# Kernel optimization log

Measured on AMD Instinct MI355X. Metric: run time of the kernel, lower is better.

The kernel has to match this reference:

```python
import jax, jax.numpy as jnp
import numpy as np

B, L, D_MODEL, D_MEM = 4, 8192, 512, 512
SSM_DIM = D_MODEL + D_MEM


def setup_inputs() -> dict:
    key = jax.random.key(0)
    ks = jax.random.split(key, 4)
    s = 0.02
    return {
        "x": jax.random.normal(ks[0], (B, L, D_MODEL), dtype=jnp.float32),
        "W_av": jax.random.normal(ks[1], (4 * D_MEM, D_MODEL), dtype=jnp.float32) * s,
        "b_av": jnp.zeros((4 * D_MEM,), dtype=jnp.float32),
        "W_go": jax.random.normal(ks[2], (D_MODEL, SSM_DIM), dtype=jnp.float32) * s,
        "b_go": jnp.zeros((D_MODEL,), dtype=jnp.float32),
        "W_out": jax.random.normal(ks[3], (2 * D_MODEL, D_MODEL), dtype=jnp.float32) * s,
        "b_out": jnp.zeros((2 * D_MODEL,), dtype=jnp.float32),
    }


def reference(x, W_av, b_av, W_go, b_go, W_out, b_out):
    d = D_MEM
    b = x.shape[0]
    # alpha_v = Linear(d_model -> 4*d_memory) on x[:, :-1]
    av = jnp.einsum("bld,kd->blk", x[:, :-1], W_av) + b_av
    # NRU memory update: alpha+*v+ - alpha-*v-  (all nonlins default to identity)
    ms_inp = av[..., :d] * av[..., d:2 * d] - av[..., 2 * d:3 * d] * av[..., 3 * d:4 * d]
    # associative cumsum scan along length, prefixed with zero initial memory
    ms = jnp.cumsum(ms_inp, axis=1)
    m_init = jnp.zeros((b, 1, d), dtype=x.dtype)
    ms = jnp.concatenate([m_init, ms], axis=1)  # [b, L, d_memory]
    ssm_inp = jnp.concatenate([x, ms], axis=2)  # [b, L, ssm_dim]
    # SSM sublayer (external registry module) stubbed as identity
    ssm_out = ssm_inp
    y = jnp.einsum("blk,dk->bld", ssm_out, W_go) + b_go  # gated_out
    y = jax.nn.gelu(y, approximate=False)  # activation='gelu' (torch exact erf)
    z = jnp.einsum("bld,kd->blk", y, W_out) + b_out  # [b, L, 2*d_model]
    y = z[..., :D_MODEL] * jax.nn.sigmoid(z[..., D_MODEL:])
    return y
```

## Files before the change

### kernel.cpp

```cpp
#include <hip/hip_runtime.h>
#include <hip/hip_bf16.h>
#include <math.h>

#define B_SZ 4
#define L_SZ 8192
#define DM 512
#define DMEM 512
#define M1 (B_SZ * (L_SZ - 1))
#define M2 (B_SZ * L_SZ)

typedef _Float16 h16;
typedef __attribute__((ext_vector_type(2))) _Float16 f16x2;
typedef __attribute__((ext_vector_type(8))) _Float16 f16x8;
typedef __attribute__((ext_vector_type(4))) float f32x4;

#define MFMA16(a, b, c) __builtin_amdgcn_mfma_f32_16x16x32_f16((a), (b), (c), 0, 0, 0)
#define WAVES_EU(mn, mx) __attribute__((amdgpu_waves_per_eu(mn, mx)))

__device__ __forceinline__ void gl16(const void* g, void* l) {
    __builtin_amdgcn_global_load_lds(
        (const __attribute__((address_space(1))) void*)g,
        (__attribute__((address_space(3))) void*)l, 16, 0, 0);
}

__device__ __forceinline__ f16x8 lds_frag(const h16* base, int row, int col, int key) {
    return *(const f16x8*)((const char*)base + row * 128 + ((col * 2) ^ (key << 4)));
}

__device__ __forceinline__ void xcd_remap(int& bx, int& by) {
    int gx = gridDim.x, gy = gridDim.y;
    int nwg = gx * gy;
    int lin = blockIdx.y * gx + blockIdx.x;
    int chunk = nwg >> 3;
    int l = (lin & 7) * chunk + (lin >> 3);
    by = l % gy;
    bx = l / gy;
}

__global__ __launch_bounds__(256) void conv_x(
    const float* __restrict__ src, h16* __restrict__ dst)
{
    int i = blockIdx.x * 256 + threadIdx.x;
    int m = i >> 6, bb = i & 63;
    const float4* s = (const float4*)(src + (size_t)m * 512 + bb * 8);
    float4 v0 = s[0], v1 = s[1];
    float vv[8] = {v0.x, v0.y, v0.z, v0.w, v1.x, v1.y, v1.z, v1.w};
    f16x8 o;
    #pragma unroll
    for (int j = 0; j < 8; ++j) o[j] = (h16)vv[j];
    int db = bb ^ (m & 7);
    *(f16x8*)(dst + (size_t)m * 512 + db * 8) = o;
}

__global__ __launch_bounds__(256) void pack_weights(
    const float* __restrict__ Wgo, const float* __restrict__ Wav,
    const float* __restrict__ Wout, h16* __restrict__ Wgoh,
    h16* __restrict__ Wavh, h16* __restrict__ Wouth)
{
    int i = blockIdx.x * 256 + threadIdx.x;
    const float* s;
    h16* d;
    if (i < 65536) {
        int r = i >> 7, bb = i & 127;
        s = Wgo + (size_t)r * 1024 + bb * 8;
        d = Wgoh + (size_t)r * 1024 + (bb ^ (r & 7)) * 8;
    } else if (i < 196608) {
        int j = i - 65536;
        int P = j >> 6, bb = j & 63;
        int by = P >> 7, lo = P & 127;
        int half = lo >> 6, g = (lo >> 4) & 3, nl = lo & 15;
        int orig = g * 512 + by * 32 + half * 16 + nl;
        s = Wav + (size_t)orig * 512 + bb * 8;
        d = Wavh + (size_t)P * 512 + (bb ^ (P & 7)) * 8;
    } else {
        int j = i - 196608;
        int P = j >> 6, bb = j & 63;
        int by = P >> 7, lo = P & 127;
        int chunk = lo >> 5, g = (lo >> 4) & 1, nl = lo & 15;
        int orig = g * 512 + by * 64 + chunk * 16 + nl;
        s = Wout + (size_t)orig * 512 + bb * 8;
        d = Wouth + (size_t)P * 512 + (bb ^ (P & 7)) * 8;
    }
    const float4* sv = (const float4*)s;
    float4 v0 = sv[0], v1 = sv[1];
    float vv[8] = {v0.x, v0.y, v0.z, v0.w, v1.x, v1.y, v1.z, v1.w};
    f16x8 hh;
    #pragma unroll
    for (int j = 0; j < 8; ++j) hh[j] = (h16)vv[j];
    *(f16x8*)d = hh;
}

#define PIPE_WAIT(N) do { \
    asm volatile("s_waitcnt vmcnt(" #N ")" ::: "memory"); \
    __builtin_amdgcn_s_barrier(); \
    asm volatile("" ::: "memory"); \
} while (0)
#define PIPE_POST() do { \
    __builtin_amdgcn_s_barrier(); \
    asm volatile("" ::: "memory"); \
} while (0)

__global__ __launch_bounds__(256) WAVES_EU(2, 2) void gemm_av_mfma(
    const h16* __restrict__ xh, const h16* __restrict__ Wh,
    const float* __restrict__ bav, float* __restrict__ ms_inp)
{
    __shared__ __align__(16) h16 As[2][128 * 64];
    __shared__ __align__(16) h16 Bh[2][128 * 64];

    int bx, by; xcd_remap(bx, by);
    const int tid = threadIdx.x, lane = tid & 63, w = tid >> 6;
    const int wm = (w & 1) * 64, wn = (w >> 1) * 64;
    const int bm = bx * 128;
    const int ln = lane & 15, ko = (lane >> 4) * 8;
    const int kb = ln & 7;
    const int wb = w * 1024;

    const char *aP[4], *hP[4];
    {
        const int r8 = lane >> 3, c16 = (lane & 7) * 16;
        #pragma unroll
        for (int i = 0; i < 4; ++i) {
            int row = i * 32 + w * 8 + r8;
            int mg = bm + row; if (mg > M1 - 1) mg = M1 - 1;
            size_t xr = (size_t)mg + (unsigned)mg / (L_SZ - 1);
            aP[i] = (const char*)xh + xr * (DM * 2) + c16;
            size_t br = (size_t)(by * 128 + row) * (DM * 2) + c16;
            hP[i] = (const char*)Wh + br;
        }
    }
    int ka[4];
    #pragma unroll
    for (int fm = 0; fm < 4; ++fm) {
        int m = bm + wm + fm * 16 + ln;
        int mg = m > M1 - 1 ? M1 - 1 : m;
        ka[fm] = (int)((mg + (unsigned)mg / (L_SZ - 1)) & 7);
    }

    f32x4 acc[4][4];
    #pragma unroll
    for (int i = 0; i < 4; ++i)
        #pragma unroll
        for (int j = 0; j < 4; ++j) acc[i][j] = (f32x4){0.f, 0.f, 0.f, 0.f};

#define STAGE_AV(koff, sel) do { \
    char* dA = (char*)As[sel]; char* dB = (char*)Bh[sel]; \
    gl16(aP[0] + (koff), dA + 0 * 4096 + wb); gl16(hP[0] + (koff), dB + 0 * 4096 + wb); \
    gl16(aP[1] + (koff), dA + 1 * 4096 + wb); gl16(hP[1] + (koff), dB + 1 * 4096 + wb); \
    gl16(aP[2] + (koff), dA + 2 * 4096 + wb); gl16(hP[2] + (koff), dB + 2 * 4096 + wb); \
    gl16(aP[3] + (koff), dA + 3 * 4096 + wb); gl16(hP[3] + (koff), dB + 3 * 4096 + wb); \
} while (0)

    STAGE_AV(0, 0);
    STAGE_AV(128, 1);
    for (int kt = 0; kt < 8; ++kt) {
        if (kt < 7) PIPE_WAIT(8); else PIPE_WAIT(0);
        const h16* A = As[kt & 1];
        const h16* B = Bh[kt & 1];
        #pragma unroll
        for (int s = 0; s < 2; ++s) {
            const int c = s * 32 + ko;
            f16x8 a[4];
            #pragma unroll
            for (int fm = 0; fm < 4; ++fm)
                a[fm] = lds_frag(A, wm + fm * 16 + ln, c, ka[fm]);
            #pragma unroll
            for (int fn = 0; fn < 4; ++fn) {
                f16x8 vh = lds_frag(B, wn + fn * 16 + ln, c, kb);
                #pragma unroll
                for (int fm = 0; fm < 4; ++fm)
                    acc[fm][fn] = MFMA16(a[fm], vh, acc[fm][fn]);
            }
        }
        PIPE_POST();
        if (kt + 2 < 8) STAGE_AV((kt + 2) * 128, kt & 1);
    }
#undef STAGE_AV

    const int lm = (lane >> 4) * 4;
    const int nn = by * 32 + (wn >> 6) * 16 + ln;
    const float b0 = bav[nn], b1 = bav[nn + 512], b2 = bav[nn + 1024], b3 = bav[nn + 1536];
    #pragma unroll
    for (int fm = 0; fm < 4; ++fm) {
        #pragma unroll
        for (int i = 0; i < 4; ++i) {
            int m = bm + wm + fm * 16 + lm + i;
            if (m < M1) {
                float a0 = acc[fm][0][i] + b0;
                float a1 = acc[fm][1][i] + b1;
                float a2 = acc[fm][2][i] + b2;
                float a3 = acc[fm][3][i] + b3;
                ms_inp[(size_t)m * DMEM + nn] = a0 * a1 - a2 * a3;
            }
        }
    }
}

__global__ __launch_bounds__(256) void scan_pass1(
    const float* __restrict__ ms_inp, float* __restrict__ csum)
{
    int c = blockIdx.x, b = blockIdx.y;
    int l0 = c * 128;
    int len = min(128, (L_SZ - 1) - l0);
    int t = threadIdx.x;
    const float2* p = (const float2*)(ms_inp + ((size_t)b * (L_SZ - 1) + l0) * DMEM) + t;
    float2 s = make_float2(0.f, 0.f);
    for (int i = 0; i < len; ++i) {
        float2 v = p[(size_t)i * 256];
        s.x += v.x; s.y += v.y;
    }
    ((float2*)(csum + ((size_t)b * 64 + c) * DMEM))[t] = s;
}

__global__ __launch_bounds__(256) void scan_pass2(float* __restrict__ csum)
{
    int sid = blockIdx.x * 4 + (threadIdx.x >> 6);
    int lane = threadIdx.x & 63;
    int b = sid >> 9, d = sid & 511;
    float* p = csum + (size_t)b * 64 * DMEM + d;
    float v = p[(size_t)lane * DMEM];
    #pragma unroll
    for (int off = 1; off < 64; off <<= 1) {
        float t = __shfl_up(v, off, 64);
        if (lane >= off) v += t;
    }
    float ex = __shfl_up(v, 1, 64);
    if (lane == 0) ex = 0.f;
    p[(size_t)lane * DMEM] = ex;
}

__global__ __launch_bounds__(256) void scan_pass3(
    const float* __restrict__ ms_inp, const float* __restrict__ csum,
    h16* __restrict__ msh)
{
    int c = blockIdx.x, b = blockIdx.y;
    int l0 = c * 128;
    int len = min(128, (L_SZ - 1) - l0);
    int t = threadIdx.x;
    float2 run = ((const float2*)(csum + ((size_t)b * 64 + c) * DMEM))[t];
    const float2* p = (const float2*)(ms_inp + ((size_t)b * (L_SZ - 1) + l0) * DMEM) + t;
    const int bb = t >> 2;
    const int sub = (t & 3) * 4;
    if (c == 0) {
        f16x2 z = {(h16)0.f, (h16)0.f};
        *(f16x2*)((char*)(msh + (size_t)b * L_SZ * DMEM) + bb * 16 + sub) = z;
    }
    for (int i = 0; i < len; ++i) {
        float2 v = p[(size_t)i * 256];
        run.x += v.x; run.y += v.y;
        int m = b * L_SZ + l0 + 1 + i;
        int db = bb ^ (m & 7);
        f16x2 o = {(h16)run.x, (h16)run.y};
        *(f16x2*)((char*)(msh + (size_t)m * DMEM) + db * 16 + sub) = o;
    }
}

__global__ __launch_bounds__(256) WAVES_EU(2, 2) void gemm_go_mfma(
    const h16* __restrict__ xh, const h16* __restrict__ msh,
    const h16* __restrict__ Wh,
    const float* __restrict__ bgo, h16* __restrict__ yh)
{
    __shared__ __align__(16) h16 As[2][128 * 64];
    __shared__ __align__(16) h16 Bh[2][128 * 64];

    int bx, by; xcd_remap(bx, by);
    const int tid = threadIdx.x, lane = tid & 63, w = tid >> 6;
    const int wm = (w & 1) * 64, wn = (w >> 1) * 64;
    const int bm = bx * 128, bn = by * 128;
    const int ln = lane & 15, ko = (lane >> 4) * 8;
    const int kk = ln & 7;
    const int wb = w * 1024;

    const char *xP[4], *mP[4], *hP[4];
    {
        const int r8 = lane >> 3, c16 = (lane & 7) * 16;
        #pragma unroll
        for (int i = 0; i < 4; ++i) {
            int row = i * 32 + w * 8 + r8;
            size_t ar = (size_t)(bm + row) * (DM * 2) + c16;
            xP[i] = (const char*)xh + ar;
            mP[i] = (const char*)msh + ar;
            size_t br = (size_t)(bn + row) * (2 * DM * 2) + c16;
            hP[i] = (const char*)Wh + br;
        }
    }

    f32x4 acc[4][4];
    #pragma unroll
    for (int i = 0; i < 4; ++i)
        #pragma unroll
        for (int j = 0; j < 4; ++j) acc[i][j] = (f32x4){0.f, 0.f, 0.f, 0.f};

#define STAGE_GO(tt, sel) do { \
    char* dA = (char*)As[sel]; char* dB = (char*)Bh[sel]; \
    const int bo = (tt) * 128; \
    if ((tt) < 8) { \
        const int ao = (tt) * 128; \
        gl16(xP[0] + ao, dA + 0 * 4096 + wb); gl16(hP[0] + bo, dB + 0 * 4096 + wb); \
        gl16(xP[1] + ao, dA + 1 * 4096 + wb); gl16(hP[1] + bo, dB + 1 * 4096 + wb); \
        gl16(xP[2] + ao, dA + 2 * 4096 + wb); gl16(hP[2] + bo, dB + 2 * 4096 + wb); \
        gl16(xP[3] + ao, dA + 3 * 4096 + wb); gl16(hP[3] + bo, dB + 3 * 4096 + wb); \
    } else { \
        const int ao = ((tt) - 8) * 128; \
        gl16(mP[0] + ao, dA + 0 * 4096 + wb); gl16(hP[0] + bo, dB + 0 * 4096 + wb); \
        gl16(mP[1] + ao, dA + 1 * 4096 + wb); gl16(hP[1] + bo, dB + 1 * 4096 + wb); \
        gl16(mP[2] + ao, dA + 2 * 4096 + wb); gl16(hP[2] + bo, dB + 2 * 4096 + wb); \
        gl16(mP[3] + ao, dA + 3 * 4096 + wb); gl16(hP[3] + bo, dB + 3 * 4096 + wb); \
    } \
} while (0)

    STAGE_GO(0, 0);
    STAGE_GO(1, 1);
    for (int kt = 0; kt < 16; ++kt) {
        if (kt < 15) PIPE_WAIT(8); else PIPE_WAIT(0);
        const h16* A = As[kt & 1];
        const h16* B = Bh[kt & 1];
        #pragma unroll
        for (int s = 0; s < 2; ++s) {
            const int c = s * 32 + ko;
            f16x8 a[4];
            #pragma unroll
            for (int fm = 0; fm < 4; ++fm)
                a[fm] = lds_frag(A, wm + fm * 16 + ln, c, kk);
            #pragma unroll
            for (int fn = 0; fn < 4; ++fn) {
                f16x8 vh = lds_frag(B, wn + fn * 16 + ln, c, kk);
                #pragma unroll
                for (int fm = 0; fm < 4; ++fm)
                    acc[fm][fn] = MFMA16(a[fm], vh, acc[fm][fn]);
            }
        }
        PIPE_POST();
        if (kt + 2 < 16) STAGE_GO(kt + 2, kt & 1);
    }
#undef STAGE_GO

    const int lm = (lane >> 4) * 4;
    #pragma unroll
    for (int fm = 0; fm < 4; ++fm) {
        #pragma unroll
        for (int fn = 0; fn < 4; ++fn) {
            int n = bn + wn + fn * 16 + ln;
            float bias = bgo[n];
            #pragma unroll
            for (int i = 0; i < 4; ++i) {
                int m = bm + wm + fm * 16 + lm + i;
                float t = acc[fm][fn][i] + bias;
                float g = 0.5f * t * (1.0f + erff(t * 0.70710678118654752f));
                int nsw = (((n >> 3) ^ (m & 7)) << 3) | (n & 7);
                yh[(size_t)m * DM + nsw] = (h16)g;
            }
        }
    }
}

__global__ __launch_bounds__(256) WAVES_EU(2, 2) void gemm_out_mfma(
    const h16* __restrict__ yh, const h16* __restrict__ Wh,
    const float* __restrict__ bout, float* __restrict__ out)
{
    __shared__ __align__(16) h16 As[2][128 * 64];
    __shared__ __align__(16) h16 Bh[2][128 * 64];

    int bx, by; xcd_remap(bx, by);
    const int tid = threadIdx.x, lane = tid & 63, w = tid >> 6;
    const int wm = (w & 1) * 64, wn = (w >> 1) * 64;
    const int bm = bx * 128;
    const int ln = lane & 15, ko = (lane >> 4) * 8;
    const int kk = ln & 7;
    const int wb = w * 1024;

    const char *aP[4], *hP[4];
    {
        const int r8 = lane >> 3, c16 = (lane & 7) * 16;
        #pragma unroll
        for (int i = 0; i < 4; ++i) {
            int row = i * 32 + w * 8 + r8;
            aP[i] = (const char*)yh + (size_t)(bm + row) * (DM * 2) + c16;
            size_t br = (size_t)(by * 128 + row) * (DM * 2) + c16;
            hP[i] = (const char*)Wh + br;
        }
    }

    f32x4 acc[4][4];
    #pragma unroll
    for (int i = 0; i < 4; ++i)
        #pragma unroll
        for (int j = 0; j < 4; ++j) acc[i][j] = (f32x4){0.f, 0.f, 0.f, 0.f};

#define STAGE_OUT(koff, sel) do { \
    char* dA = (char*)As[sel]; char* dB = (char*)Bh[sel]; \
    gl16(aP[0] + (koff), dA + 0 * 4096 + wb); gl16(hP[0] + (koff), dB + 0 * 4096 + wb); \
    gl16(aP[1] + (koff), dA + 1 * 4096 + wb); gl16(hP[1] + (koff), dB + 1 * 4096 + wb); \
    gl16(aP[2] + (koff), dA + 2 * 4096 + wb); gl16(hP[2] + (koff), dB + 2 * 4096 + wb); \
    gl16(aP[3] + (koff), dA + 3 * 4096 + wb); gl16(hP[3] + (koff), dB + 3 * 4096 + wb); \
} while (0)

    STAGE_OUT(0, 0);
    STAGE_OUT(128, 1);
    for (int kt = 0; kt < 8; ++kt) {
        if (kt < 7) PIPE_WAIT(8); else PIPE_WAIT(0);
        const h16* A = As[kt & 1];
        const h16* B = Bh[kt & 1];
        #pragma unroll
        for (int s = 0; s < 2; ++s) {
            const int c = s * 32 + ko;
            f16x8 a[4];
            #pragma unroll
            for (int fm = 0; fm < 4; ++fm)
                a[fm] = lds_frag(A, wm + fm * 16 + ln, c, kk);
            #pragma unroll
            for (int fn = 0; fn < 4; ++fn) {
                f16x8 vh = lds_frag(B, wn + fn * 16 + ln, c, kk);
                #pragma unroll
                for (int fm = 0; fm < 4; ++fm)
                    acc[fm][fn] = MFMA16(a[fm], vh, acc[fm][fn]);
            }
        }
        PIPE_POST();
        if (kt + 2 < 8) STAGE_OUT((kt + 2) * 128, kt & 1);
    }
#undef STAGE_OUT

    const int lm = (lane >> 4) * 4;
    #pragma unroll
    for (int fm = 0; fm < 4; ++fm) {
        #pragma unroll
        for (int cp = 0; cp < 2; ++cp) {
            int ncol = by * 64 + ((wn >> 5) + cp) * 16 + ln;
            float bz0 = bout[ncol], bz1 = bout[ncol + 512];
            #pragma unroll
            for (int i = 0; i < 4; ++i) {
                int m = bm + wm + fm * 16 + lm + i;
                float z0 = acc[fm][cp * 2 + 0][i] + bz0;
                float z1 = acc[fm][cp * 2 + 1][i] + bz1;
                out[(size_t)m * DM + ncol] = z0 * (1.0f / (1.0f + expf(-z1)));
            }
        }
    }
}

extern "C" void kernel_launch(void* const* d_in, const int* in_sizes, int n_in,
                              void* d_out, int out_size, void* d_ws, size_t ws_size,
                              hipStream_t stream)
{
    const float* x    = (const float*)d_in[0];
    const float* Wav  = (const float*)d_in[1];
    const float* bav  = (const float*)d_in[2];
    const float* Wgo  = (const float*)d_in[3];
    const float* bgo  = (const float*)d_in[4];
    const float* Wout = (const float*)d_in[5];
    const float* bout = (const float*)d_in[6];
    float* out = (float*)d_out;

    char* ws = (char*)d_ws;
    const size_t MB = 1 << 20;
    float* ms_inp = (float*)ws;
    h16*   yh     = (h16*)ws;
    h16*   xh     = (h16*)(ws + 64 * MB);
    h16*   msh    = (h16*)(ws + 96 * MB);
    float* csum   = (float*)(ws + 128 * MB);
    h16*   Wavh   = (h16*)(ws + 129 * MB);
    h16*   Wgoh   = (h16*)(ws + 131 * MB);
    h16*   Wouth  = (h16*)(ws + 132 * MB);

    conv_x      <<<8192, 256, 0, stream>>>(x, xh);
    pack_weights<<<1024, 256, 0, stream>>>(Wgo, Wav, Wout, Wgoh, Wavh, Wouth);
    gemm_av_mfma<<<dim3(256, 16), 256, 0, stream>>>(xh, Wavh, bav, ms_inp);
    scan_pass1<<<dim3(64, B_SZ), 256, 0, stream>>>(ms_inp, csum);
    scan_pass2<<<512, 256, 0, stream>>>(csum);
    scan_pass3<<<dim3(64, B_SZ), 256, 0, stream>>>(ms_inp, csum, msh);
    gemm_go_mfma<<<dim3(256, 4), 256, 0, stream>>>(xh, msh, Wgoh, bgo, yh);
    gemm_out_mfma<<<dim3(256, 8), 256, 0, stream>>>(yh, Wouth, bout, out);
}
```

Before: 277.2 us.

## Store ms_inp in fp16, fuse prep kernels, single-buffer av GEMM at 3 waves

The memory-update intermediate ms_inp is now written in fp16 instead of fp32, which halves traffic for the av GEMM epilogue and both scan passes. The scans are reworked so that one wave handles a chunk with 8-wide vector loads and stores. The x conversion and weight packing are merged into a single launch. The av GEMM drops LDS double buffering so that three waves per EU fit, which trades load/compute overlap for occupancy and adds fp16 rounding of the scan inputs.

After: 275.8 us. Within noise of the previous version (-0.5%).

```diff
diff --git a/kernel.cpp b/kernel.cpp
--- a/kernel.cpp
+++ b/kernel.cpp
@@ -37,49 +37,42 @@
     bx = l / gy;
 }
 
-__global__ __launch_bounds__(256) void conv_x(
-    const float* __restrict__ src, h16* __restrict__ dst)
-{
-    int i = blockIdx.x * 256 + threadIdx.x;
-    int m = i >> 6, bb = i & 63;
-    const float4* s = (const float4*)(src + (size_t)m * 512 + bb * 8);
-    float4 v0 = s[0], v1 = s[1];
-    float vv[8] = {v0.x, v0.y, v0.z, v0.w, v1.x, v1.y, v1.z, v1.w};
-    f16x8 o;
-    #pragma unroll
-    for (int j = 0; j < 8; ++j) o[j] = (h16)vv[j];
-    int db = bb ^ (m & 7);
-    *(f16x8*)(dst + (size_t)m * 512 + db * 8) = o;
-}
-
-__global__ __launch_bounds__(256) void pack_weights(
-    const float* __restrict__ Wgo, const float* __restrict__ Wav,
-    const float* __restrict__ Wout, h16* __restrict__ Wgoh,
+__global__ __launch_bounds__(256) void prep_all(
+    const float* __restrict__ x, const float* __restrict__ Wgo,
+    const float* __restrict__ Wav, const float* __restrict__ Wout,
+    h16* __restrict__ xh, h16* __restrict__ Wgoh,
     h16* __restrict__ Wavh, h16* __restrict__ Wouth)
 {
     int i = blockIdx.x * 256 + threadIdx.x;
     const float* s;
     h16* d;
-    if (i < 65536) {
-        int r = i >> 7, bb = i & 127;
-        s = Wgo + (size_t)r * 1024 + bb * 8;
-        d = Wgoh + (size_t)r * 1024 + (bb ^ (r & 7)) * 8;
-    } else if (i < 196608) {
-        int j = i - 65536;
-        int P = j >> 6, bb = j & 63;
-        int by = P >> 7, lo = P & 127;
-        int half = lo >> 6, g = (lo >> 4) & 3, nl = lo & 15;
-        int orig = g * 512 + by * 32 + half * 16 + nl;
-        s = Wav + (size_t)orig * 512 + bb * 8;
-        d = Wavh + (size_t)P * 512 + (bb ^ (P & 7)) * 8;
+    if (i < 2097152) {
+        int m = i >> 6, bb = i & 63;
+        s = x + (size_t)m * 512 + bb * 8;
+        d = xh + (size_t)m * 512 + (bb ^ (m & 7)) * 8;
     } else {
-        int j = i - 196608;
-        int P = j >> 6, bb = j & 63;
-        int by = P >> 7, lo = P & 127;
-        int chunk = lo >> 5, g = (lo >> 4) & 1, nl = lo & 15;
-        int orig = g * 512 + by * 64 + chunk * 16 + nl;
-        s = Wout + (size_t)orig * 512 + bb * 8;
-        d = Wouth + (size_t)P * 512 + (bb ^ (P & 7)) * 8;
+        int j = i - 2097152;
+        if (j < 65536) {
+            int r = j >> 7, bb = j & 127;
+            s = Wgo + (size_t)r * 1024 + bb * 8;
+            d = Wgoh + (size_t)r * 1024 + (bb ^ (r & 7)) * 8;
+        } else if (j < 196608) {
+            int k = j - 65536;
+            int P = k >> 6, bb = k & 63;
+            int by = P >> 7, lo = P & 127;
+            int half = lo >> 6, g = (lo >> 4) & 3, nl = lo & 15;
+            int orig = g * 512 + by * 32 + half * 16 + nl;
+            s = Wav + (size_t)orig * 512 + bb * 8;
+            d = Wavh + (size_t)P * 512 + (bb ^ (P & 7)) * 8;
+        } else {
+            int k = j - 196608;
+            int P = k >> 6, bb = k & 63;
+            int by = P >> 7, lo = P & 127;
+            int chunk = lo >> 5, g = (lo >> 4) & 1, nl = lo & 15;
+            int orig = g * 512 + by * 64 + chunk * 16 + nl;
+            s = Wout + (size_t)orig * 512 + bb * 8;
+            d = Wouth + (size_t)P * 512 + (bb ^ (P & 7)) * 8;
+        }
     }
     const float4* sv = (const float4*)s;
     float4 v0 = sv[0], v1 = sv[1];
@@ -100,12 +93,12 @@
     asm volatile("" ::: "memory"); \
 } while (0)
 
-__global__ __launch_bounds__(256) WAVES_EU(2, 2) void gemm_av_mfma(
+__global__ __launch_bounds__(256) WAVES_EU(3, 3) void gemm_av_mfma(
     const h16* __restrict__ xh, const h16* __restrict__ Wh,
-    const float* __restrict__ bav, float* __restrict__ ms_inp)
-{
-    __shared__ __align__(16) h16 As[2][128 * 64];
-    __shared__ __align__(16) h16 Bh[2][128 * 64];
+    const float* __restrict__ bav, h16* __restrict__ ms_inp)
+{
+    __shared__ __align__(16) h16 As[128 * 64];
+    __shared__ __align__(16) h16 Bh[128 * 64];
 
     int bx, by; xcd_remap(bx, by);
     const int tid = threadIdx.x, lane = tid & 63, w = tid >> 6;
@@ -113,6 +106,7 @@
     const int bm = bx * 128;
     const int ln = lane & 15, ko = (lane >> 4) * 8;
     const int kb = ln & 7;
+    char* lA = (char*)As; char* lH = (char*)Bh;
     const int wb = w * 1024;
 
     const char *aP[4], *hP[4];
@@ -142,37 +136,34 @@
         #pragma unroll
         for (int j = 0; j < 4; ++j) acc[i][j] = (f32x4){0.f, 0.f, 0.f, 0.f};
 
-#define STAGE_AV(koff, sel) do { \
-    char* dA = (char*)As[sel]; char* dB = (char*)Bh[sel]; \
-    gl16(aP[0] + (koff), dA + 0 * 4096 + wb); gl16(hP[0] + (koff), dB + 0 * 4096 + wb); \
-    gl16(aP[1] + (koff), dA + 1 * 4096 + wb); gl16(hP[1] + (koff), dB + 1 * 4096 + wb); \
-    gl16(aP[2] + (koff), dA + 2 * 4096 + wb); gl16(hP[2] + (koff), dB + 2 * 4096 + wb); \
-    gl16(aP[3] + (koff), dA + 3 * 4096 + wb); gl16(hP[3] + (koff), dB + 3 * 4096 + wb); \
+#define STAGE_AV(koff) do { \
+    gl16(aP[0] + (koff), lA + 0 * 4096 + wb); gl16(hP[0] + (koff), lH + 0 * 4096 + wb); \
+    gl16(aP[1] + (koff), lA + 1 * 4096 + wb); gl16(hP[1] + (koff), lH + 1 * 4096 + wb); \
+    gl16(aP[2] + (koff), lA + 2 * 4096 + wb); gl16(hP[2] + (koff), lH + 2 * 4096 + wb); \
+    gl16(aP[3] + (koff), lA + 3 * 4096 + wb); gl16(hP[3] + (koff), lH + 3 * 4096 + wb); \
 } while (0)
 
-    STAGE_AV(0, 0);
-    STAGE_AV(128, 1);
+    STAGE_AV(0);
     for (int kt = 0; kt < 8; ++kt) {
-        if (kt < 7) PIPE_WAIT(8); else PIPE_WAIT(0);
-        const h16* A = As[kt & 1];
-        const h16* B = Bh[kt & 1];
+        asm volatile("s_waitcnt vmcnt(0)" ::: "memory");
+        __syncthreads();
         #pragma unroll
         for (int s = 0; s < 2; ++s) {
             const int c = s * 32 + ko;
             f16x8 a[4];
             #pragma unroll
             for (int fm = 0; fm < 4; ++fm)
-                a[fm] = lds_frag(A, wm + fm * 16 + ln, c, ka[fm]);
+                a[fm] = lds_frag(As, wm + fm * 16 + ln, c, ka[fm]);
             #pragma unroll
             for (int fn = 0; fn < 4; ++fn) {
-                f16x8 vh = lds_frag(B, wn + fn * 16 + ln, c, kb);
+                f16x8 vh = lds_frag(Bh, wn + fn * 16 + ln, c, kb);
                 #pragma unroll
                 for (int fm = 0; fm < 4; ++fm)
                     acc[fm][fn] = MFMA16(a[fm], vh, acc[fm][fn]);
             }
         }
-        PIPE_POST();
-        if (kt + 2 < 8) STAGE_AV((kt + 2) * 128, kt & 1);
+        __syncthreads();
+        if (kt < 7) STAGE_AV((kt + 1) * 128);
     }
 #undef STAGE_AV
 
@@ -189,26 +180,30 @@
                 float a1 = acc[fm][1][i] + b1;
                 float a2 = acc[fm][2][i] + b2;
                 float a3 = acc[fm][3][i] + b3;
-                ms_inp[(size_t)m * DMEM + nn] = a0 * a1 - a2 * a3;
+                ms_inp[(size_t)m * DMEM + nn] = (h16)(a0 * a1 - a2 * a3);
             }
         }
     }
 }
 
 __global__ __launch_bounds__(256) void scan_pass1(
-    const float* __restrict__ ms_inp, float* __restrict__ csum)
-{
-    int c = blockIdx.x, b = blockIdx.y;
+    const h16* __restrict__ ms_inp, float* __restrict__ csum)
+{
+    int b = blockIdx.y;
+    int c = blockIdx.x * 4 + (threadIdx.x >> 6);
+    int t = threadIdx.x & 63;
     int l0 = c * 128;
     int len = min(128, (L_SZ - 1) - l0);
-    int t = threadIdx.x;
-    const float2* p = (const float2*)(ms_inp + ((size_t)b * (L_SZ - 1) + l0) * DMEM) + t;
-    float2 s = make_float2(0.f, 0.f);
+    const h16* p = ms_inp + ((size_t)b * (L_SZ - 1) + l0) * DMEM + t * 8;
+    float s[8] = {0.f, 0.f, 0.f, 0.f, 0.f, 0.f, 0.f, 0.f};
     for (int i = 0; i < len; ++i) {
-        float2 v = p[(size_t)i * 256];
-        s.x += v.x; s.y += v.y;
-    }
-    ((float2*)(csum + ((size_t)b * 64 + c) * DMEM))[t] = s;
+        f16x8 v = *(const f16x8*)(p + (size_t)i * DMEM);
+        #pragma unroll
+        for (int j = 0; j < 8; ++j) s[j] += (float)v[j];
+    }
+    float* q = csum + ((size_t)b * 64 + c) * DMEM + t * 8;
+    *(float4*)q       = make_float4(s[0], s[1], s[2], s[3]);
+    *(float4*)(q + 4) = make_float4(s[4], s[5], s[6], s[7]);
 }
 
 __global__ __launch_bounds__(256) void scan_pass2(float* __restrict__ csum)
@@ -229,28 +224,31 @@
 }
 
 __global__ __launch_bounds__(256) void scan_pass3(
-    const float* __restrict__ ms_inp, const float* __restrict__ csum,
+    const h16* __restrict__ ms_inp, const float* __restrict__ csum,
     h16* __restrict__ msh)
 {
-    int c = blockIdx.x, b = blockIdx.y;
+    int b = blockIdx.y;
+    int c = blockIdx.x * 4 + (threadIdx.x >> 6);
+    int t = threadIdx.x & 63;
     int l0 = c * 128;
     int len = min(128, (L_SZ - 1) - l0);
-    int t = threadIdx.x;
-    float2 run = ((const float2*)(csum + ((size_t)b * 64 + c) * DMEM))[t];
-    const float2* p = (const float2*)(ms_inp + ((size_t)b * (L_SZ - 1) + l0) * DMEM) + t;
-    const int bb = t >> 2;
-    const int sub = (t & 3) * 4;
+    const float* q = csum + ((size_t)b * 64 + c) * DMEM + t * 8;
+    float run[8];
+    #pragma unroll
+    for (int j = 0; j < 8; ++j) run[j] = q[j];
+    const h16* p = ms_inp + ((size_t)b * (L_SZ - 1) + l0) * DMEM + t * 8;
     if (c == 0) {
-        f16x2 z = {(h16)0.f, (h16)0.f};
-        *(f16x2*)((char*)(msh + (size_t)b * L_SZ * DMEM) + bb * 16 + sub) = z;
+        f16x8 z = {};
+        *(f16x8*)(msh + (size_t)b * L_SZ * DMEM + t * 8) = z;
     }
     for (int i = 0; i < len; ++i) {
-        float2 v = p[(size_t)i * 256];
-        run.x += v.x; run.y += v.y;
+        f16x8 v = *(const f16x8*)(p + (size_t)i * DMEM);
+        f16x8 o;
+        #pragma unroll
+        for (int j = 0; j < 8; ++j) { run[j] += (float)v[j]; o[j] = (h16)run[j]; }
         int m = b * L_SZ + l0 + 1 + i;
-        int db = bb ^ (m & 7);
-        f16x2 o = {(h16)run.x, (h16)run.y};
-        *(f16x2*)((char*)(msh + (size_t)m * DMEM) + db * 16 + sub) = o;
+        int db = t ^ (m & 7);
+        *(f16x8*)(msh + (size_t)m * DMEM + db * 8) = o;
     }
 }
 
@@ -453,8 +451,8 @@
 
     char* ws = (char*)d_ws;
     const size_t MB = 1 << 20;
-    float* ms_inp = (float*)ws;
-    h16*   yh     = (h16*)ws;
+    h16*   ms_inp = (h16*)ws;
+    h16*   yh     = (h16*)(ws + 32 * MB);
     h16*   xh     = (h16*)(ws + 64 * MB);
     h16*   msh    = (h16*)(ws + 96 * MB);
     float* csum   = (float*)(ws + 128 * MB);
@@ -462,12 +460,11 @@
     h16*   Wgoh   = (h16*)(ws + 131 * MB);
     h16*   Wouth  = (h16*)(ws + 132 * MB);
 
-    conv_x      <<<8192, 256, 0, stream>>>(x, xh);
-    pack_weights<<<1024, 256, 0, stream>>>(Wgo, Wav, Wout, Wgoh, Wavh, Wouth);
+    prep_all<<<9216, 256, 0, stream>>>(x, Wgo, Wav, Wout, xh, Wgoh, Wavh, Wouth);
     gemm_av_mfma<<<dim3(256, 16), 256, 0, stream>>>(xh, Wavh, bav, ms_inp);
-    scan_pass1<<<dim3(64, B_SZ), 256, 0, stream>>>(ms_inp, csum);
+    scan_pass1<<<dim3(16, B_SZ), 256, 0, stream>>>(ms_inp, csum);
     scan_pass2<<<512, 256, 0, stream>>>(csum);
-    scan_pass3<<<dim3(64, B_SZ), 256, 0, stream>>>(ms_inp, csum, msh);
+    scan_pass3<<<dim3(16, B_SZ), 256, 0, stream>>>(ms_inp, csum, msh);
     gemm_go_mfma<<<dim3(256, 4), 256, 0, stream>>>(xh, msh, Wgoh, bgo, yh);
     gemm_out_mfma<<<dim3(256, 8), 256, 0, stream>>>(yh, Wouth, bout, out);
 }
```
